# Kernel tuning notes

Measured on AMD Instinct MI355X. Metric: run time of the kernel, lower is better.

Reference implementation:

```python
import jax, jax.numpy as jnp
import numpy as np

NUM_CLASSES = 1000
FEAT_DIM = 512
BATCH = 65536


def setup_inputs() -> dict:
    key = jax.random.key(0)
    k1, k2, k3 = jax.random.split(key, 3)
    features = jax.random.normal(k1, (BATCH, FEAT_DIM), dtype=jnp.float32)
    centers = jax.random.normal(k2, (NUM_CLASSES, FEAT_DIM), dtype=jnp.float32)
    labels = jax.random.randint(k3, (BATCH,), 0, NUM_CLASSES, dtype=jnp.int64)
    return {"features": features, "centers": centers, "labels": labels}


def reference(features, centers, labels):
    # Torch loop: for each class j with count>0, add F.mse_loss(z_j, center_j)
    # = sum_{i: l_i=j} ||f_i - c_j||^2 / (count_j * feat_dim); final /= batch_size.
    batch_size, feat_dim = features.shape
    num_classes = centers.shape[0]
    labels = labels.astype(jnp.int32)
    c = jax.lax.stop_gradient(centers)  # centers are detached in the original
    # per-sample squared distance to its own class center: [batch]
    diff = features - c[labels]
    d = jnp.sum(diff * diff, axis=-1)
    # per-class sums and counts in one segment-reduce pass
    sums = jax.ops.segment_sum(d, labels, num_segments=num_classes)
    counts = jax.ops.segment_sum(jnp.ones_like(d), labels, num_segments=num_classes)
    per_class = jnp.where(counts > 0, sums / (counts * feat_dim), 0.0)
    return jnp.sum(per_class) / batch_size
```

## Files before the change

kernel.cpp:

```cpp
#include <hip/hip_runtime.h>


#define WAVE 64
#define CPAD 1024
#define MAX_COPIES 64

__global__ __launch_bounds__(256) void center_dist_kernel(
    const float* __restrict__ features,
    const float* __restrict__ centers,
    const int*   __restrict__ labels,
    float* __restrict__ ws,
    int batch, int feat, int ncopy)
{
    const int wave_in_block = threadIdx.x >> 6;
    const int lane          = threadIdx.x & 63;
    const int wave_id       = blockIdx.x * 4 + wave_in_block;
    if (wave_id >= batch) return;
    const int sample        = wave_id;

    const int label = labels[sample];

    float* __restrict__ my = ws + (size_t)(wave_id & (ncopy - 1)) * (2 * CPAD);

    const float4* __restrict__ f4 =
        (const float4*)(features + (size_t)sample * feat);
    const float4* __restrict__ c4 =
        (const float4*)(centers + (size_t)label * feat);

    float acc = 0.0f;
    const int n4 = feat >> 2;
#pragma unroll 2
    for (int idx = lane; idx < n4; idx += WAVE) {
        float4 fv = f4[idx];
        float4 cv = c4[idx];
        float dx = fv.x - cv.x;
        float dy = fv.y - cv.y;
        float dz = fv.z - cv.z;
        float dw = fv.w - cv.w;
        acc += dx * dx + dy * dy;
        acc += dz * dz + dw * dw;
    }

#pragma unroll
    for (int off = 32; off > 0; off >>= 1)
        acc += __shfl_down(acc, off, WAVE);

    if (lane == 0) {
        atomicAdd(&my[label], acc);
        atomicAdd(&my[CPAD + label], 1.0f);
    }
}

__global__ __launch_bounds__(1024) void center_finalize_kernel(
    const float* __restrict__ ws,
    float* __restrict__ out,
    int nclass, int feat, int batch, int ncopy)
{
    const int j = threadIdx.x;
    float term = 0.0f;
    if (j < nclass) {
        float s = 0.0f;
        float n = 0.0f;
#pragma unroll 4
        for (int c = 0; c < ncopy; ++c) {
            const float* __restrict__ cp = ws + (size_t)c * (2 * CPAD);
            s += cp[j];
            n += cp[CPAD + j];
        }
        if (n > 0.0f) term = s / (n * (float)feat);
    }

#pragma unroll
    for (int off = 32; off > 0; off >>= 1)
        term += __shfl_down(term, off, WAVE);

    __shared__ float warp_part[16];
    const int lane = threadIdx.x & 63;
    const int wid  = threadIdx.x >> 6;
    if (lane == 0) warp_part[wid] = term;
    __syncthreads();

    if (threadIdx.x < WAVE) {
        float v = (threadIdx.x < 16) ? warp_part[threadIdx.x] : 0.0f;
#pragma unroll
        for (int off = 8; off > 0; off >>= 1)
            v += __shfl_down(v, off, WAVE);
        if (threadIdx.x == 0) out[0] = v / (float)batch;
    }
}

extern "C" void kernel_launch(void* const* d_in, const int* in_sizes, int n_in,
                              void* d_out, int out_size, void* d_ws, size_t ws_size,
                              hipStream_t stream) {
    const float* features = (const float*)d_in[0];
    const float* centers  = (const float*)d_in[1];
    const int*   labels   = (const int*)d_in[2];

    const int batch  = in_sizes[2];
    const int feat   = in_sizes[0] / batch;
    const int nclass = in_sizes[1] / feat;

    const size_t copy_bytes = (size_t)(2 * CPAD) * sizeof(float);
    int ncopy = MAX_COPIES;
    while (ncopy > 1 && (size_t)ncopy * copy_bytes > ws_size) ncopy >>= 1;

    hipMemsetAsync(d_ws, 0, (size_t)ncopy * copy_bytes, stream);

    const int blocks = (batch + 3) / 4;
    center_dist_kernel<<<blocks, 256, 0, stream>>>(
        features, centers, labels, (float*)d_ws, batch, feat, ncopy);

    center_finalize_kernel<<<1, 1024, 0, stream>>>(
        (const float*)d_ws, (float*)d_out, nclass, feat, batch, ncopy);
}
```

Baseline: 205.4 us.

## Replace per-class global atomics with per-sample distances, label histogram, and weighted reduction

The distance kernel now writes each sample's squared distance to a buffer instead of atomically adding sums and counts into replicated per-class slots. Class counts are built by a separate shared-memory histogram kernel, turned into inverse counts, and a single-block final kernel sums distance times inverse count over all samples. This removes global float atomics and the workspace memset, but adds two extra launches and a serial single-block pass over 65536 samples.

```diff
diff --git a/kernel.cpp b/kernel.cpp
--- a/kernel.cpp
+++ b/kernel.cpp
@@ -2,25 +2,21 @@
 
 
 #define WAVE 64
-#define CPAD 1024
-#define MAX_COPIES 64
+#define HPAD 1024
 
 __global__ __launch_bounds__(256) void center_dist_kernel(
     const float* __restrict__ features,
     const float* __restrict__ centers,
     const int*   __restrict__ labels,
-    float* __restrict__ ws,
-    int batch, int feat, int ncopy)
+    float* __restrict__ dvals,
+    int batch, int feat)
 {
     const int wave_in_block = threadIdx.x >> 6;
     const int lane          = threadIdx.x & 63;
-    const int wave_id       = blockIdx.x * 4 + wave_in_block;
-    if (wave_id >= batch) return;
-    const int sample        = wave_id;
+    const int sample        = blockIdx.x * 4 + wave_in_block;
+    if (sample >= batch) return;
 
     const int label = labels[sample];
-
-    float* __restrict__ my = ws + (size_t)(wave_id & (ncopy - 1)) * (2 * CPAD);
 
     const float4* __restrict__ f4 =
         (const float4*)(features + (size_t)sample * feat);
@@ -45,39 +41,62 @@
     for (int off = 32; off > 0; off >>= 1)
         acc += __shfl_down(acc, off, WAVE);
 
-    if (lane == 0) {
-        atomicAdd(&my[label], acc);
-        atomicAdd(&my[CPAD + label], 1.0f);
+    if (lane == 0) dvals[sample] = acc;
+}
+
+__global__ __launch_bounds__(256) void hist_kernel(
+    const int* __restrict__ labels,
+    unsigned int* __restrict__ hist,
+    int batch, int nclass)
+{
+    __shared__ unsigned int h[HPAD];
+    for (int j = threadIdx.x; j < HPAD; j += 256) h[j] = 0u;
+    __syncthreads();
+
+    const int base = blockIdx.x * 1024;
+    for (int k = threadIdx.x; k < 1024; k += 256) {
+        const int i = base + k;
+        if (i < batch) atomicAdd(&h[labels[i]], 1u);
+    }
+    __syncthreads();
+
+    unsigned int* __restrict__ out = hist + (size_t)blockIdx.x * HPAD;
+    for (int j = threadIdx.x; j < nclass; j += 256) out[j] = h[j];
+}
+
+__global__ __launch_bounds__(1024) void counts_kernel(
+    const unsigned int* __restrict__ hist,
+    float* __restrict__ invcnt,
+    int nclass, int feat, int nblocks)
+{
+    for (int j = threadIdx.x; j < nclass; j += 1024) {
+        unsigned int n = 0;
+#pragma unroll 4
+        for (int b = 0; b < nblocks; ++b)
+            n += hist[(size_t)b * HPAD + j];
+        invcnt[j] = (n > 0u) ? 1.0f / ((float)n * (float)feat) : 0.0f;
     }
 }
 
-__global__ __launch_bounds__(1024) void center_finalize_kernel(
-    const float* __restrict__ ws,
+__global__ __launch_bounds__(1024) void final_kernel(
+    const float* __restrict__ dvals,
+    const int*   __restrict__ labels,
+    const float* __restrict__ invcnt,
     float* __restrict__ out,
-    int nclass, int feat, int batch, int ncopy)
+    int batch)
 {
-    const int j = threadIdx.x;
-    float term = 0.0f;
-    if (j < nclass) {
-        float s = 0.0f;
-        float n = 0.0f;
-#pragma unroll 4
-        for (int c = 0; c < ncopy; ++c) {
-            const float* __restrict__ cp = ws + (size_t)c * (2 * CPAD);
-            s += cp[j];
-            n += cp[CPAD + j];
-        }
-        if (n > 0.0f) term = s / (n * (float)feat);
-    }
+    float acc = 0.0f;
+    for (int i = threadIdx.x; i < batch; i += 1024)
+        acc += dvals[i] * invcnt[labels[i]];
 
 #pragma unroll
     for (int off = 32; off > 0; off >>= 1)
-        term += __shfl_down(term, off, WAVE);
+        acc += __shfl_down(acc, off, WAVE);
 
     __shared__ float warp_part[16];
     const int lane = threadIdx.x & 63;
     const int wid  = threadIdx.x >> 6;
-    if (lane == 0) warp_part[wid] = term;
+    if (lane == 0) warp_part[wid] = acc;
     __syncthreads();
 
     if (threadIdx.x < WAVE) {
@@ -100,16 +119,19 @@
     const int feat   = in_sizes[0] / batch;
     const int nclass = in_sizes[1] / feat;
 
-    const size_t copy_bytes = (size_t)(2 * CPAD) * sizeof(float);
-    int ncopy = MAX_COPIES;
-    while (ncopy > 1 && (size_t)ncopy * copy_bytes > ws_size) ncopy >>= 1;
+    const int nblocks_h = (batch + 1023) / 1024;
 
-    hipMemsetAsync(d_ws, 0, (size_t)ncopy * copy_bytes, stream);
+    float*        dvals  = (float*)d_ws;
+    unsigned int* hist   = (unsigned int*)(dvals + batch);
+    float*        invcnt = (float*)(hist + (size_t)nblocks_h * HPAD);
 
-    const int blocks = (batch + 3) / 4;
-    center_dist_kernel<<<blocks, 256, 0, stream>>>(
-        features, centers, labels, (float*)d_ws, batch, feat, ncopy);
+    center_dist_kernel<<<(batch + 3) / 4, 256, 0, stream>>>(
+        features, centers, labels, dvals, batch, feat);
 
-    center_finalize_kernel<<<1, 1024, 0, stream>>>(
-        (const float*)d_ws, (float*)d_out, nclass, feat, batch, ncopy);
+    hist_kernel<<<nblocks_h, 256, 0, stream>>>(labels, hist, batch, nclass);
+
+    counts_kernel<<<1, 1024, 0, stream>>>(hist, invcnt, nclass, feat, nblocks_h);
+
+    final_kernel<<<1, 1024, 0, stream>>>(dvals, labels, invcnt,
+                                         (float*)d_out, batch);
 }
```

Result: slower. 230.7 us (+12.3%).
